# Performance work log

Hardware: AMD Instinct MI355X
Metric: run time of the kernel (lower is better)

## Reference

```python
import jax, jax.numpy as jnp
import numpy as np


def hard_sigmoid(x):
    # Keras hard_sigmoid: clip(0.2*x + 0.5, 0, 1)
    return jnp.clip(0.2 * x + 0.5, 0.0, 1.0)


def setup_inputs() -> dict:
    key = jax.random.key(0)
    k1, k2, k3, k4, k5 = jax.random.split(key, 5)
    B, D, U = 8192, 1024, 1024
    return {
        "inputs": jax.random.normal(k1, (B, D), dtype=jnp.float32),
        "h_tm1": jax.random.normal(k2, (B, U), dtype=jnp.float32),
        "kernel": jax.random.normal(k3, (D, 3 * U), dtype=jnp.float32) * 0.02,
        "recurrent_kernel": jax.random.normal(k4, (U, 3 * U), dtype=jnp.float32) * 0.02,
        "bias": jax.random.normal(k5, (2, 3 * U), dtype=jnp.float32) * 0.02,
    }


def reference(inputs, h_tm1, kernel, recurrent_kernel, bias):
    units = recurrent_kernel.shape[0]
    input_bias, recurrent_bias = bias[0], bias[1]

    # [B, 3U] input projection
    matrix_x = inputs @ kernel + input_bias
    x_z, x_r, x_h = jnp.split(matrix_x, 3, axis=-1)

    # [B, 3U] recurrent projection
    matrix_inner = h_tm1 @ recurrent_kernel + recurrent_bias
    rec_z = matrix_inner[:, :units]
    rec_r = matrix_inner[:, units:2 * units]
    rec_h = matrix_inner[:, 2 * units:]

    z = hard_sigmoid(x_z + rec_z)
    r = hard_sigmoid(x_r + rec_r)
    hh = jnp.tanh(x_h + r * rec_h)
    h = z * h_tm1 + (1.0 - z) * hh
    return h
```

## Files before the change

### kernel.cpp

```cpp
#include <hip/hip_runtime.h>
#include <math.h>

typedef __attribute__((ext_vector_type(4))) float floatx4;
typedef __attribute__((ext_vector_type(8))) short shortx8;

#define M_TILE 128
#define N_TILE 64
#define BK 64

__device__ __forceinline__ unsigned short f2bf(float f) {
    union { float f; unsigned int u; } v; v.f = f;
    unsigned int r = v.u + 0x7fffu + ((v.u >> 16) & 1u);
    return (unsigned short)(r >> 16);
}
__device__ __forceinline__ float bf2f(unsigned short u) {
    union { unsigned int u; float f; } v; v.u = ((unsigned int)u) << 16;
    return v.f;
}
__device__ __forceinline__ void gload_lds16(const unsigned short* g, unsigned short* l) {
    __builtin_amdgcn_global_load_lds(
        (const __attribute__((address_space(1))) void*)g,
        (__attribute__((address_space(3))) void*)l, 16, 0, 0);
}

__global__ void prep_kernel(const float* __restrict__ X, const float* __restrict__ H,
                            const float* __restrict__ W, const float* __restrict__ R,
                            unsigned short* __restrict__ Xb, unsigned short* __restrict__ Hb,
                            unsigned short* __restrict__ Wt, unsigned short* __restrict__ Rt)
{
    const int bid = blockIdx.x;
    const int tx  = threadIdx.x;
    if (bid < 16384) {
        const float* src = (bid < 8192) ? X : H;
        unsigned short* dst = (bid < 8192) ? Xb : Hb;
        const int i = (bid & 8191) * 256 + tx;
        float4 v = ((const float4*)src)[i];
        ushort4 s;
        s.x = f2bf(v.x); s.y = f2bf(v.y); s.z = f2bf(v.z); s.w = f2bf(v.w);
        ((ushort4*)dst)[i] = s;
        return;
    }
    __shared__ float tile[64][66];
    const int tb = bid - 16384;
    const float* src = (tb < 768) ? W : R;
    unsigned short* dst = (tb < 768) ? Wt : Rt;
    const int tt = (tb < 768) ? tb : tb - 768;
    const int col0 = (tt % 48) * 64;
    const int k0   = (tt / 48) * 64;
    const int n4 = tx & 15, kl = tx >> 4;
    #pragma unroll
    for (int i = 0; i < 4; ++i) {
        const int k = kl + i * 16;
        float4 v = *(const float4*)(src + (size_t)(k0 + k) * 3072 + col0 + n4 * 4);
        tile[k][n4 * 4 + 0] = v.x; tile[k][n4 * 4 + 1] = v.y;
        tile[k][n4 * 4 + 2] = v.z; tile[k][n4 * 4 + 3] = v.w;
    }
    __syncthreads();
    #pragma unroll
    for (int i = 0; i < 2; ++i) {
        const int c  = tx + i * 256;
        const int nl = c >> 3, kc = c & 7;
        ushort4 s0, s1;
        s0.x = f2bf(tile[kc*8+0][nl]); s0.y = f2bf(tile[kc*8+1][nl]);
        s0.z = f2bf(tile[kc*8+2][nl]); s0.w = f2bf(tile[kc*8+3][nl]);
        s1.x = f2bf(tile[kc*8+4][nl]); s1.y = f2bf(tile[kc*8+5][nl]);
        s1.z = f2bf(tile[kc*8+6][nl]); s1.w = f2bf(tile[kc*8+7][nl]);
        unsigned short* p = dst + (size_t)(col0 + nl) * 1024 + k0 + kc * 8;
        *(ushort4*)p = s0;
        *(ushort4*)(p + 4) = s1;
    }
}

__global__ __launch_bounds__(256, 2)
void gru_mfma_kernel(const unsigned short* __restrict__ Xb,
                     const unsigned short* __restrict__ Hb,
                     const unsigned short* __restrict__ Wt,
                     const unsigned short* __restrict__ Rt,
                     const float* __restrict__ bias,
                     float* __restrict__ out)
{
    __shared__ __attribute__((aligned(16))) unsigned short ldsA[2][M_TILE * BK];
    __shared__ __attribute__((aligned(16))) unsigned short ldsW[6][N_TILE * BK];

    const int tid  = threadIdx.x;
    const int bid  = blockIdx.x;
    const int bn   = bid & 15;
    const int bm   = bid >> 4;
    const int m0   = bm * M_TILE;
    const int n0   = bn * N_TILE;

    const int wid  = tid >> 6;
    const int lane = tid & 63;
    const int wr   = wid >> 1;
    const int wc   = wid & 1;
    const int lo   = lane & 15;
    const int quad = lane >> 4;
    const int lx   = lane & 7;

    const int lrow = lane >> 3;
    const int lkc  = (lane & 7) ^ lrow;

    floatx4 acc_z[4][2]  = {};
    floatx4 acc_r[4][2]  = {};
    floatx4 acc_xh[4][2] = {};
    floatx4 acc_rh[4][2] = {};

    for (int k0 = 0; k0 < 1024; k0 += BK) {
        #pragma unroll
        for (int r = 0; r < 8; ++r) {
            const int seg = r * 4 + wid;
            const int arr = seg >> 4;
            const int s   = seg & 15;
            const size_t gofs = (size_t)(m0 + s * 8 + lrow) * 1024 + k0 + lkc * 8;
            gload_lds16(((arr == 0) ? Xb : Hb) + gofs, &ldsA[arr][s * 512]);
        }
        #pragma unroll
        for (int r = 0; r < 12; ++r) {
            const int seg = r * 4 + wid;
            const int g   = seg >> 3;
            const int s   = seg & 7;
            const unsigned short* base = (g < 3) ? Wt : Rt;
            const int gm = (g < 3) ? g : g - 3;
            const size_t gofs = (size_t)(gm * 1024 + n0 + s * 8 + lrow) * 1024 + k0 + lkc * 8;
            gload_lds16(base + gofs, &ldsW[g][s * 512]);
        }
        __syncthreads();

        #pragma unroll
        for (int ks = 0; ks < 2; ++ks) {
            const int kcp = ((ks * 4 + quad) ^ lx) * 8;
            shortx8 a_in[4], a_h[4];
            #pragma unroll
            for (int i = 0; i < 4; ++i) {
                const int row = wr * 64 + i * 16 + lo;
                a_in[i] = *(const shortx8*)&ldsA[0][row * BK + kcp];
                a_h[i]  = *(const shortx8*)&ldsA[1][row * BK + kcp];
            }
            #pragma unroll
            for (int j = 0; j < 2; ++j) {
                const int nc = (wc * 32 + j * 16 + lo) * BK + kcp;
                shortx8 bz  = *(const shortx8*)&ldsW[0][nc];
                shortx8 bre = *(const shortx8*)&ldsW[1][nc];
                shortx8 bh  = *(const shortx8*)&ldsW[2][nc];
                shortx8 rz  = *(const shortx8*)&ldsW[3][nc];
                shortx8 rre = *(const shortx8*)&ldsW[4][nc];
                shortx8 rh  = *(const shortx8*)&ldsW[5][nc];
                #pragma unroll
                for (int i = 0; i < 4; ++i) {
                    acc_z[i][j]  = __builtin_amdgcn_mfma_f32_16x16x32_bf16(a_in[i], bz,  acc_z[i][j],  0, 0, 0);
                    acc_z[i][j]  = __builtin_amdgcn_mfma_f32_16x16x32_bf16(a_h[i],  rz,  acc_z[i][j],  0, 0, 0);
                    acc_r[i][j]  = __builtin_amdgcn_mfma_f32_16x16x32_bf16(a_in[i], bre, acc_r[i][j],  0, 0, 0);
                    acc_r[i][j]  = __builtin_amdgcn_mfma_f32_16x16x32_bf16(a_h[i],  rre, acc_r[i][j],  0, 0, 0);
                    acc_xh[i][j] = __builtin_amdgcn_mfma_f32_16x16x32_bf16(a_in[i], bh,  acc_xh[i][j], 0, 0, 0);
                    acc_rh[i][j] = __builtin_amdgcn_mfma_f32_16x16x32_bf16(a_h[i],  rh,  acc_rh[i][j], 0, 0, 0);
                }
            }
        }
        __syncthreads();
    }

    #pragma unroll
    for (int j = 0; j < 2; ++j) {
        const int col = n0 + wc * 32 + j * 16 + lo;
        const float bz  = bias[col]        + bias[3072 + col];
        const float brr = bias[1024 + col] + bias[4096 + col];
        const float b0h = bias[2048 + col];
        const float b1h = bias[5120 + col];
        #pragma unroll
        for (int i = 0; i < 4; ++i) {
            const int rowb = m0 + wr * 64 + i * 16 + quad * 4;
            #pragma unroll
            for (int r = 0; r < 4; ++r) {
                const int row = rowb + r;
                float sz = acc_z[i][j][r]  + bz;
                float sr = acc_r[i][j][r]  + brr;
                float xh = acc_xh[i][j][r] + b0h;
                float rh = acc_rh[i][j][r] + b1h;
                float z   = fminf(fmaxf(0.2f * sz + 0.5f, 0.0f), 1.0f);
                float rr2 = fminf(fmaxf(0.2f * sr + 0.5f, 0.0f), 1.0f);
                float pre = xh + rr2 * rh;
                float e   = __expf(2.0f * pre);
                float th  = 1.0f - 2.0f / (e + 1.0f);
                float hp  = bf2f(Hb[(size_t)row * 1024 + col]);
                out[(size_t)row * 1024 + col] = z * hp + (1.0f - z) * th;
            }
        }
    }
}

#define KP 40
#define FBK 32
__global__ __launch_bounds__(256, 2)
void gru_fused_kernel(const float* __restrict__ X, const float* __restrict__ H,
                      const float* __restrict__ W, const float* __restrict__ R,
                      const float* __restrict__ bias, float* __restrict__ out)
{
    __shared__ __attribute__((aligned(16))) unsigned short ldsA[2][M_TILE * KP];
    __shared__ __attribute__((aligned(16))) unsigned short ldsW[6][N_TILE * KP];
    const int tid = threadIdx.x, bid = blockIdx.x;
    const int bn = bid & 15, bm = bid >> 4;
    const int m0 = bm * M_TILE, n0 = bn * N_TILE;
    const int wid = tid >> 6, lane = tid & 63;
    const int wr = wid >> 1, wc = wid & 1;
    const int lo = lane & 15, quad = lane >> 4;
    floatx4 acc_z[4][2] = {}, acc_r[4][2] = {}, acc_xh[4][2] = {}, acc_rh[4][2] = {};
    for (int k0 = 0; k0 < 1024; k0 += FBK) {
        #pragma unroll
        for (int i = 0; i < 8; ++i) {
            int idx = tid + i * 256;
            const float* base = (idx < 1024) ? X : H;
            int rem = idx & 1023, row = rem >> 3, kq = rem & 7;
            const float4 v = *(const float4*)(base + (size_t)(m0 + row) * 1024 + k0 + kq * 4);
            ushort4 s; s.x = f2bf(v.x); s.y = f2bf(v.y); s.z = f2bf(v.z); s.w = f2bf(v.w);
            *(ushort4*)&ldsA[idx >> 10][row * KP + kq * 4] = s;
        }
        #pragma unroll
        for (int i = 0; i < 3; ++i) {
            int b = tid + i * 256, g = b >> 7, rem = b & 127, kb = rem >> 4, c4 = rem & 15;
            const float* wb = (g < 3) ? W : R;
            int gm = (g < 3) ? g : g - 3;
            const float* src = wb + (size_t)(k0 + kb * 4) * 3072 + gm * 1024 + n0 + c4 * 4;
            float4 r0 = *(const float4*)(src);
            float4 r1 = *(const float4*)(src + 3072);
            float4 r2 = *(const float4*)(src + 2 * 3072);
            float4 r3 = *(const float4*)(src + 3 * 3072);
            ushort4 s0, s1, s2, s3;
            s0.x=f2bf(r0.x); s0.y=f2bf(r1.x); s0.z=f2bf(r2.x); s0.w=f2bf(r3.x);
            s1.x=f2bf(r0.y); s1.y=f2bf(r1.y); s1.z=f2bf(r2.y); s1.w=f2bf(r3.y);
            s2.x=f2bf(r0.z); s2.y=f2bf(r1.z); s2.z=f2bf(r2.z); s2.w=f2bf(r3.z);
            s3.x=f2bf(r0.w); s3.y=f2bf(r1.w); s3.z=f2bf(r2.w); s3.w=f2bf(r3.w);
            unsigned short* dst = &ldsW[g][0];
            *(ushort4*)&dst[(c4*4+0)*KP + kb*4] = s0;
            *(ushort4*)&dst[(c4*4+1)*KP + kb*4] = s1;
            *(ushort4*)&dst[(c4*4+2)*KP + kb*4] = s2;
            *(ushort4*)&dst[(c4*4+3)*KP + kb*4] = s3;
        }
        __syncthreads();
        shortx8 a_in[4], a_h[4];
        #pragma unroll
        for (int i = 0; i < 4; ++i) {
            a_in[i] = *(const shortx8*)&ldsA[0][(wr*64 + i*16 + lo) * KP + quad*8];
            a_h[i]  = *(const shortx8*)&ldsA[1][(wr*64 + i*16 + lo) * KP + quad*8];
        }
        #pragma unroll
        for (int j = 0; j < 2; ++j) {
            const int nc = (wc*32 + j*16 + lo) * KP + quad*8;
            shortx8 bz  = *(const shortx8*)&ldsW[0][nc];
            shortx8 bre = *(const shortx8*)&ldsW[1][nc];
            shortx8 bh  = *(const shortx8*)&ldsW[2][nc];
            shortx8 rz  = *(const shortx8*)&ldsW[3][nc];
            shortx8 rre = *(const shortx8*)&ldsW[4][nc];
            shortx8 rh  = *(const shortx8*)&ldsW[5][nc];
            #pragma unroll
            for (int i = 0; i < 4; ++i) {
                acc_z[i][j]  = __builtin_amdgcn_mfma_f32_16x16x32_bf16(a_in[i], bz,  acc_z[i][j],  0, 0, 0);
                acc_z[i][j]  = __builtin_amdgcn_mfma_f32_16x16x32_bf16(a_h[i],  rz,  acc_z[i][j],  0, 0, 0);
                acc_r[i][j]  = __builtin_amdgcn_mfma_f32_16x16x32_bf16(a_in[i], bre, acc_r[i][j],  0, 0, 0);
                acc_r[i][j]  = __builtin_amdgcn_mfma_f32_16x16x32_bf16(a_h[i],  rre, acc_r[i][j],  0, 0, 0);
                acc_xh[i][j] = __builtin_amdgcn_mfma_f32_16x16x32_bf16(a_in[i], bh,  acc_xh[i][j], 0, 0, 0);
                acc_rh[i][j] = __builtin_amdgcn_mfma_f32_16x16x32_bf16(a_h[i],  rh,  acc_rh[i][j], 0, 0, 0);
            }
        }
        __syncthreads();
    }
    #pragma unroll
    for (int j = 0; j < 2; ++j) {
        const int col = n0 + wc*32 + j*16 + lo;
        const float bz  = bias[col]        + bias[3072 + col];
        const float brr = bias[1024 + col] + bias[4096 + col];
        const float b0h = bias[2048 + col];
        const float b1h = bias[5120 + col];
        #pragma unroll
        for (int i = 0; i < 4; ++i) {
            const int rowb = m0 + wr*64 + i*16 + quad*4;
            #pragma unroll
            for (int r = 0; r < 4; ++r) {
                const int row = rowb + r;
                float sz = acc_z[i][j][r]  + bz;
                float sr = acc_r[i][j][r]  + brr;
                float xh = acc_xh[i][j][r] + b0h;
                float rh = acc_rh[i][j][r] + b1h;
                float z   = fminf(fmaxf(0.2f * sz + 0.5f, 0.0f), 1.0f);
                float rr2 = fminf(fmaxf(0.2f * sr + 0.5f, 0.0f), 1.0f);
                float pre = xh + rr2 * rh;
                float e   = __expf(2.0f * pre);
                float th  = 1.0f - 2.0f / (e + 1.0f);
                float hp  = H[(size_t)row * 1024 + col];
                out[(size_t)row * 1024 + col] = z * hp + (1.0f - z) * th;
            }
        }
    }
}

extern "C" void kernel_launch(void* const* d_in, const int* in_sizes, int n_in,
                              void* d_out, int out_size, void* d_ws, size_t ws_size,
                              hipStream_t stream)
{
    const float* X    = (const float*)d_in[0];
    const float* H    = (const float*)d_in[1];
    const float* W    = (const float*)d_in[2];
    const float* R    = (const float*)d_in[3];
    const float* bias = (const float*)d_in[4];
    float* out = (float*)d_out;

    const size_t need = (size_t)(8192 * 1024) * 2 * 2 + (size_t)(3072 * 1024) * 2 * 2;
    if (ws_size >= need) {
        unsigned short* Xb = (unsigned short*)d_ws;
        unsigned short* Hb = Xb + (size_t)8192 * 1024;
        unsigned short* Wt = Hb + (size_t)8192 * 1024;
        unsigned short* Rt = Wt + (size_t)3072 * 1024;
        hipLaunchKernelGGL(prep_kernel, dim3(16384 + 1536), dim3(256), 0, stream,
                           X, H, W, R, Xb, Hb, Wt, Rt);
        hipLaunchKernelGGL(gru_mfma_kernel, dim3(1024), dim3(256), 0, stream,
                           Xb, Hb, Wt, Rt, bias, out);
    } else {
        hipLaunchKernelGGL(gru_fused_kernel, dim3(1024), dim3(256), 0, stream, X, H, W, R, bias, out);
    }
}
```

Measured before the change: 228.6 us.

## Double-buffer activation tiles in LDS and read weights directly from global

Drops the LDS staging of the six weight tiles. Each lane now loads its B fragments straight from global memory, relying on the cache for reuse across the two row-waves. The activation tiles are double-buffered in LDS, and the next K-slice is prefetched during compute, removing one barrier per iteration. The risk is that global weight loads sit on the MFMA critical path with high latency, and the weights are fetched redundantly by the waves that share them.

```diff
diff --git a/kernel.cpp b/kernel.cpp
--- a/kernel.cpp
+++ b/kernel.cpp
@@ -79,8 +79,7 @@
                      const float* __restrict__ bias,
                      float* __restrict__ out)
 {
-    __shared__ __attribute__((aligned(16))) unsigned short ldsA[2][M_TILE * BK];
-    __shared__ __attribute__((aligned(16))) unsigned short ldsW[6][N_TILE * BK];
+    __shared__ __attribute__((aligned(16))) unsigned short ldsA[2][2][M_TILE * BK];
 
     const int tid  = threadIdx.x;
     const int bid  = blockIdx.x;
@@ -100,31 +99,41 @@
     const int lrow = lane >> 3;
     const int lkc  = (lane & 7) ^ lrow;
 
+    const int ncol = n0 + wc * 32 + lo;
+    const unsigned short* pWz = Wt + (size_t)(       ncol) * 1024;
+    const unsigned short* pWr = Wt + (size_t)(1024 + ncol) * 1024;
+    const unsigned short* pWh = Wt + (size_t)(2048 + ncol) * 1024;
+    const unsigned short* pRz = Rt + (size_t)(       ncol) * 1024;
+    const unsigned short* pRr = Rt + (size_t)(1024 + ncol) * 1024;
+    const unsigned short* pRh = Rt + (size_t)(2048 + ncol) * 1024;
+
     floatx4 acc_z[4][2]  = {};
     floatx4 acc_r[4][2]  = {};
     floatx4 acc_xh[4][2] = {};
     floatx4 acc_rh[4][2] = {};
 
+    #pragma unroll
+    for (int r = 0; r < 8; ++r) {
+        const int seg = r * 4 + wid;
+        const int arr = seg >> 4;
+        const int s   = seg & 15;
+        const size_t gofs = (size_t)(m0 + s * 8 + lrow) * 1024 + lkc * 8;
+        gload_lds16(((arr == 0) ? Xb : Hb) + gofs, &ldsA[0][arr][s * 512]);
+    }
+    __syncthreads();
+
+    int p = 0;
     for (int k0 = 0; k0 < 1024; k0 += BK) {
-        #pragma unroll
-        for (int r = 0; r < 8; ++r) {
-            const int seg = r * 4 + wid;
-            const int arr = seg >> 4;
-            const int s   = seg & 15;
-            const size_t gofs = (size_t)(m0 + s * 8 + lrow) * 1024 + k0 + lkc * 8;
-            gload_lds16(((arr == 0) ? Xb : Hb) + gofs, &ldsA[arr][s * 512]);
-        }
-        #pragma unroll
-        for (int r = 0; r < 12; ++r) {
-            const int seg = r * 4 + wid;
-            const int g   = seg >> 3;
-            const int s   = seg & 7;
-            const unsigned short* base = (g < 3) ? Wt : Rt;
-            const int gm = (g < 3) ? g : g - 3;
-            const size_t gofs = (size_t)(gm * 1024 + n0 + s * 8 + lrow) * 1024 + k0 + lkc * 8;
-            gload_lds16(base + gofs, &ldsW[g][s * 512]);
-        }
-        __syncthreads();
+        if (k0 + BK < 1024) {
+            #pragma unroll
+            for (int r = 0; r < 8; ++r) {
+                const int seg = r * 4 + wid;
+                const int arr = seg >> 4;
+                const int s   = seg & 15;
+                const size_t gofs = (size_t)(m0 + s * 8 + lrow) * 1024 + (k0 + BK) + lkc * 8;
+                gload_lds16(((arr == 0) ? Xb : Hb) + gofs, &ldsA[p ^ 1][arr][s * 512]);
+            }
+        }
 
         #pragma unroll
         for (int ks = 0; ks < 2; ++ks) {
@@ -133,18 +142,19 @@
             #pragma unroll
             for (int i = 0; i < 4; ++i) {
                 const int row = wr * 64 + i * 16 + lo;
-                a_in[i] = *(const shortx8*)&ldsA[0][row * BK + kcp];
-                a_h[i]  = *(const shortx8*)&ldsA[1][row * BK + kcp];
-            }
+                a_in[i] = *(const shortx8*)&ldsA[p][0][row * BK + kcp];
+                a_h[i]  = *(const shortx8*)&ldsA[p][1][row * BK + kcp];
+            }
+            const size_t ko = (size_t)(k0 + ks * 32 + quad * 8);
             #pragma unroll
             for (int j = 0; j < 2; ++j) {
-                const int nc = (wc * 32 + j * 16 + lo) * BK + kcp;
-                shortx8 bz  = *(const shortx8*)&ldsW[0][nc];
-                shortx8 bre = *(const shortx8*)&ldsW[1][nc];
-                shortx8 bh  = *(const shortx8*)&ldsW[2][nc];
-                shortx8 rz  = *(const shortx8*)&ldsW[3][nc];
-                shortx8 rre = *(const shortx8*)&ldsW[4][nc];
-                shortx8 rh  = *(const shortx8*)&ldsW[5][nc];
+                const size_t bo = (size_t)j * 16384 + ko;
+                shortx8 bz  = *(const shortx8*)(pWz + bo);
+                shortx8 bre = *(const shortx8*)(pWr + bo);
+                shortx8 bh  = *(const shortx8*)(pWh + bo);
+                shortx8 rz  = *(const shortx8*)(pRz + bo);
+                shortx8 rre = *(const shortx8*)(pRr + bo);
+                shortx8 rh  = *(const shortx8*)(pRh + bo);
                 #pragma unroll
                 for (int i = 0; i < 4; ++i) {
                     acc_z[i][j]  = __builtin_amdgcn_mfma_f32_16x16x32_bf16(a_in[i], bz,  acc_z[i][j],  0, 0, 0);
@@ -157,6 +167,7 @@
             }
         }
         __syncthreads();
+        p ^= 1;
     }
 
     #pragma unroll
```

After: 325.2 us. 42.3% more time.
